# Kernel optimization log

Measured on AMD Instinct MI355X. Metric: run time of the kernel, lower is better.

Reference implementation:

```python
import jax, jax.numpy as jnp
import numpy as np

# NF4 codebook (bitsandbytes nf4 quant_type), 16 levels in [-1, 1]
NF4 = jnp.array([
    -1.0, -0.6961928009986877, -0.5250730514526367, -0.39491748809814453,
    -0.28444138169288635, -0.18477343022823334, -0.09105003625154495, 0.0,
    0.07958029955625534, 0.16093020141124725, 0.24611230194568634,
    0.33791524171829224, 0.44070982933044434, 0.5626170039176941,
    0.7229568362236023, 1.0], dtype=jnp.float32)
BLOCK = 64  # bitsandbytes default quant block size

TOKENS, HD, M = 8192, 4096, 11008


def dequant_nf4(codes, scales):
    # codes: [out, in] int in [0,16); scales: [out, in//BLOCK] per-block absmax
    out_f, in_f = codes.shape
    w = NF4[codes].reshape(out_f, in_f // BLOCK, BLOCK) * scales[:, :, None]
    return w.reshape(out_f, in_f)


def setup_inputs() -> dict:
    key = jax.random.key(0)
    k = jax.random.split(key, 7)
    return {
        "x": jax.random.normal(k[0], (TOKENS, HD), dtype=jnp.float32),
        "gate_codes": jax.random.randint(k[1], (M, HD), 0, 16, dtype=jnp.int32),
        "gate_scales": jax.random.uniform(k[2], (M, HD // BLOCK), dtype=jnp.float32) * 0.1,
        "up_codes": jax.random.randint(k[3], (M, HD), 0, 16, dtype=jnp.int32),
        "up_scales": jax.random.uniform(k[4], (M, HD // BLOCK), dtype=jnp.float32) * 0.1,
        "down_codes": jax.random.randint(k[5], (HD, M), 0, 16, dtype=jnp.int32),
        "down_scales": jax.random.uniform(k[6], (HD, M // BLOCK), dtype=jnp.float32) * 0.1,
    }


def reference(x, gate_codes, gate_scales, up_codes, up_scales, down_codes, down_scales):
    Wg = dequant_nf4(gate_codes, gate_scales)   # [m, hd]
    Wu = dequant_nf4(up_codes, up_scales)       # [m, hd]
    Wd = dequant_nf4(down_codes, down_scales)   # [hd, m]
    g = jnp.einsum('td,md->tm', x, Wg)          # gate_proj(x)
    u = jnp.einsum('td,md->tm', x, Wu)          # up_proj(x)
    h = jax.nn.silu(g) * u                      # SwiGLU
    return jnp.einsum('tm,dm->td', h, Wd)       # down_proj
```

## Files before the change

### kernel.cpp

```cpp
#include <hip/hip_runtime.h>
#include <hip/hip_bf16.h>

typedef _Float16 half8 __attribute__((ext_vector_type(8)));
typedef float floatx4 __attribute__((ext_vector_type(4)));

__device__ __constant__ float NF4_TAB[16] = {
    -1.0f, -0.6961928009986877f, -0.5250730514526367f, -0.39491748809814453f,
    -0.28444138169288635f, -0.18477343022823334f, -0.09105003625154495f, 0.0f,
    0.07958029955625534f, 0.16093020141124725f, 0.24611230194568634f,
    0.33791524171829224f, 0.44070982933044434f, 0.5626170039176941f,
    0.7229568362236023f, 1.0f};

typedef __attribute__((address_space(3))) void lds_t;
typedef __attribute__((address_space(1))) void gbl_t;

__device__ __forceinline__ void gload16(const void* g, void* l) {
  __builtin_amdgcn_global_load_lds((gbl_t*)g, (lds_t*)l, 16, 0, 0);
}

#define FENCE() asm volatile("" ::: "memory")

__global__ void cvt_f32_to_f16_pad(const float* __restrict__ in,
                                   _Float16* __restrict__ out,
                                   int total8, int C8, int OS) {
  int stride = gridDim.x * blockDim.x;
  for (int i = blockIdx.x * blockDim.x + threadIdx.x; i < total8; i += stride) {
    int row = i / C8;
    int col = (i - row * C8) * 8;
    const float4* ip = reinterpret_cast<const float4*>(in + (long)row * (C8 * 8) + col);
    float4 a = ip[0], b = ip[1];
    half8 o;
    o[0] = (_Float16)a.x; o[1] = (_Float16)a.y;
    o[2] = (_Float16)a.z; o[3] = (_Float16)a.w;
    o[4] = (_Float16)b.x; o[5] = (_Float16)b.y;
    o[6] = (_Float16)b.z; o[7] = (_Float16)b.w;
    *reinterpret_cast<half8*>(out + (long)row * OS + col) = o;
  }
}

__global__ void dequant_nf4(const int* __restrict__ codes,
                            const float* __restrict__ scales,
                            _Float16* __restrict__ out,
                            int total8, int C, int CB, int OS) {
  __shared__ float lut[16];
  if (threadIdx.x < 16) lut[threadIdx.x] = NF4_TAB[threadIdx.x];
  __syncthreads();
  int stride = gridDim.x * blockDim.x;
  for (int i = blockIdx.x * blockDim.x + threadIdx.x; i < total8; i += stride) {
    long e = (long)i * 8;
    int row = (int)(e / C);
    int col = (int)(e - (long)row * C);
    float sc = scales[row * CB + (col >> 6)];
    const int4* cp = reinterpret_cast<const int4*>(codes + e);
    int4 c0 = cp[0];
    int4 c1 = cp[1];
    half8 o;
    o[0] = (_Float16)(lut[c0.x & 15] * sc);
    o[1] = (_Float16)(lut[c0.y & 15] * sc);
    o[2] = (_Float16)(lut[c0.z & 15] * sc);
    o[3] = (_Float16)(lut[c0.w & 15] * sc);
    o[4] = (_Float16)(lut[c1.x & 15] * sc);
    o[5] = (_Float16)(lut[c1.y & 15] * sc);
    o[6] = (_Float16)(lut[c1.z & 15] * sc);
    o[7] = (_Float16)(lut[c1.w & 15] * sc);
    *reinterpret_cast<half8*>(out + (long)row * OS + col) = o;
  }
}

template <int K, int LD, int N, int EPI>
__global__ __launch_bounds__(512, 2) void gemm256(
    const _Float16* __restrict__ A,
    const _Float16* __restrict__ B,
    _Float16* __restrict__ GH,
    float* __restrict__ OUT) {
  constexpr int NT = K / 64;
  constexpr int NBC = N / 256;
  __shared__ __align__(16) _Float16 lds[2 * 32768];

  const int t = threadIdx.x;
  const int lane = t & 63;
  const int wave = t >> 6;
  const int wm = wave >> 2;
  const int wn = wave & 3;

  const int xcd = blockIdx.x & 7;
  const int j = blockIdx.x >> 3;
  const int bm = 4 * xcd + (j & 3);
  const int bn = j >> 2;

  const int lc = (t & 3) ^ ((t >> 3) & 3);
  const _Float16* gA = A + ((long)bm * 256 + (t >> 2)) * LD + lc * 8;
  const _Float16* gB = B + ((long)bn * 256 + (t >> 2)) * LD + lc * 8;
  const long rstep = (long)128 * LD;
  const int dst = t * 8;

  const int rA = wm * 128 + (lane & 15);
  const int rB = wn * 64 + (lane & 15);
  const int ckA = ((lane >> 4) ^ ((rA >> 1) & 3)) * 8;
  const int ckB = ((lane >> 4) ^ ((rB >> 1) & 3)) * 8;
  const int offA = rA * 32 + ckA;
  const int offB = 16384 + rB * 32 + ckB;

#define STAGE_SLOT(gp, slab, koff, dbuf)                                   \
  gload16((gp) + (koff), lds + (dbuf) * 32768 + (slab) + dst);             \
  gload16((gp) + (koff) + rstep, lds + (dbuf) * 32768 + (slab) + dst + 4096);

  STAGE_SLOT(gA, 0, 0, 0);
  STAGE_SLOT(gB, 16384, 0, 0);
  STAGE_SLOT(gA, 8192, 32, 0);
  STAGE_SLOT(gB, 24576, 32, 0);
  gA += 64; gB += 64;
  asm volatile("s_waitcnt vmcnt(4)" ::: "memory");
  __builtin_amdgcn_s_barrier();
  FENCE();

  floatx4 acc[8][4] = {};

  for (int kt = 0; kt < NT; ++kt) {
    const int cb = kt & 1;
    const int sbuf = cb ^ 1;
    const _Float16* lb = lds + cb * 32768;
    const bool st = (kt + 1 < NT);
    const bool last = (kt == NT - 1);

    half8 a[8], b[2];

#pragma unroll
    for (int i = 0; i < 8; ++i)
      a[i] = *reinterpret_cast<const half8*>(&lb[offA + i * 512]);
    b[0] = *reinterpret_cast<const half8*>(&lb[offB]);
    b[1] = *reinterpret_cast<const half8*>(&lb[offB + 512]);
    if (st) { STAGE_SLOT(gA, 0, 0, sbuf); }
    __builtin_amdgcn_s_barrier();
    FENCE();
    __builtin_amdgcn_s_setprio(1);
#pragma unroll
    for (int i = 0; i < 8; ++i) {
      acc[i][0] = __builtin_amdgcn_mfma_f32_16x16x32_f16(a[i], b[0], acc[i][0], 0, 0, 0);
      acc[i][1] = __builtin_amdgcn_mfma_f32_16x16x32_f16(a[i], b[1], acc[i][1], 0, 0, 0);
    }
    __builtin_amdgcn_s_setprio(0);
    __builtin_amdgcn_s_barrier();
    FENCE();

    b[0] = *reinterpret_cast<const half8*>(&lb[offB + 2 * 512]);
    b[1] = *reinterpret_cast<const half8*>(&lb[offB + 3 * 512]);
    if (st) { STAGE_SLOT(gB, 16384, 0, sbuf); }
    if (last) { asm volatile("s_waitcnt vmcnt(0)" ::: "memory"); }
    else      { asm volatile("s_waitcnt vmcnt(4)" ::: "memory"); }
    __builtin_amdgcn_s_barrier();
    FENCE();
    __builtin_amdgcn_s_setprio(1);
#pragma unroll
    for (int i = 0; i < 8; ++i) {
      acc[i][2] = __builtin_amdgcn_mfma_f32_16x16x32_f16(a[i], b[0], acc[i][2], 0, 0, 0);
      acc[i][3] = __builtin_amdgcn_mfma_f32_16x16x32_f16(a[i], b[1], acc[i][3], 0, 0, 0);
    }
    __builtin_amdgcn_s_setprio(0);
    __builtin_amdgcn_s_barrier();
    FENCE();

#pragma unroll
    for (int i = 0; i < 8; ++i)
      a[i] = *reinterpret_cast<const half8*>(&lb[8192 + offA + i * 512]);
    b[0] = *reinterpret_cast<const half8*>(&lb[8192 + offB]);
    b[1] = *reinterpret_cast<const half8*>(&lb[8192 + offB + 512]);
    if (st) { STAGE_SLOT(gA, 8192, 32, sbuf); }
    __builtin_amdgcn_s_barrier();
    FENCE();
    __builtin_amdgcn_s_setprio(1);
#pragma unroll
    for (int i = 0; i < 8; ++i) {
      acc[i][0] = __builtin_amdgcn_mfma_f32_16x16x32_f16(a[i], b[0], acc[i][0], 0, 0, 0);
      acc[i][1] = __builtin_amdgcn_mfma_f32_16x16x32_f16(a[i], b[1], acc[i][1], 0, 0, 0);
    }
    __builtin_amdgcn_s_setprio(0);
    __builtin_amdgcn_s_barrier();
    FENCE();

    b[0] = *reinterpret_cast<const half8*>(&lb[8192 + offB + 2 * 512]);
    b[1] = *reinterpret_cast<const half8*>(&lb[8192 + offB + 3 * 512]);
    if (st) { STAGE_SLOT(gB, 24576, 32, sbuf); gA += 64; gB += 64; }
    if (!last) { asm volatile("s_waitcnt vmcnt(4)" ::: "memory"); }
    __builtin_amdgcn_s_barrier();
    FENCE();
    __builtin_amdgcn_s_setprio(1);
#pragma unroll
    for (int i = 0; i < 8; ++i) {
      acc[i][2] = __builtin_amdgcn_mfma_f32_16x16x32_f16(a[i], b[0], acc[i][2], 0, 0, 0);
      acc[i][3] = __builtin_amdgcn_mfma_f32_16x16x32_f16(a[i], b[1], acc[i][3], 0, 0, 0);
    }
    __builtin_amdgcn_s_setprio(0);
    __builtin_amdgcn_s_barrier();
    FENCE();
  }
#undef STAGE_SLOT

  const int r0 = bm * 256 + wm * 128 + (lane >> 4) * 4;
  const int c0 = bn * 256 + wn * 64 + (lane & 15);

  if (EPI == 1) {
    _Float16* lg = lds;
    const _Float16* gsrc = GH + (long)(bm * 256) * N + bn * 256;
#pragma unroll
    for (int r = 0; r < 16; ++r) {
      const int row = r * 16 + (t >> 5);
      const int col = (t & 31) * 8;
      gload16(gsrc + (long)row * N + col, lg + r * 4096 + t * 8);
    }
    asm volatile("s_waitcnt vmcnt(0)" ::: "memory");
    __builtin_amdgcn_s_barrier();
    FENCE();
    const int lr0 = wm * 128 + (lane >> 4) * 4;
    const int lc0 = wn * 64 + (lane & 15);
#pragma unroll
    for (int i = 0; i < 8; ++i) {
#pragma unroll
      for (int j2 = 0; j2 < 4; ++j2) {
#pragma unroll
        for (int ii = 0; ii < 4; ++ii) {
          const long idx = (long)(r0 + i * 16 + ii) * N + (c0 + j2 * 16);
          float u = acc[i][j2][ii];
          float g = (float)lg[(lr0 + i * 16 + ii) * 256 + (lc0 + j2 * 16)];
          GH[idx] = (_Float16)(g / (1.0f + __expf(-g)) * u);
        }
      }
    }
  } else {
#pragma unroll
    for (int i = 0; i < 8; ++i) {
#pragma unroll
      for (int j2 = 0; j2 < 4; ++j2) {
#pragma unroll
        for (int ii = 0; ii < 4; ++ii) {
          const long idx = (long)(r0 + i * 16 + ii) * N + (c0 + j2 * 16);
          if (EPI == 0) {
            GH[idx] = (_Float16)acc[i][j2][ii];
          } else {
            OUT[idx] = acc[i][j2][ii];
          }
        }
      }
    }
  }
}

extern "C" void kernel_launch(void* const* d_in, const int* in_sizes, int n_in,
                              void* d_out, int out_size, void* d_ws, size_t ws_size,
                              hipStream_t stream) {
  const float* x           = (const float*)d_in[0];
  const int*   gate_codes  = (const int*)d_in[1];
  const float* gate_scales = (const float*)d_in[2];
  const int*   up_codes    = (const int*)d_in[3];
  const float* up_scales   = (const float*)d_in[4];
  const int*   down_codes  = (const int*)d_in[5];
  const float* down_scales = (const float*)d_in[6];
  float* out = (float*)d_out;

  const long T = 8192, HD = 4096, M = 11008;
  const long LDP = 4160;

  char* ws = (char*)d_ws;
  _Float16* x16 = (_Float16*)ws;
  _Float16* W   = (_Float16*)(ws + T * LDP * 2);
  _Float16* gh  = (_Float16*)(ws + T * LDP * 2 + M * LDP * 2);

  cvt_f32_to_f16_pad<<<2048, 256, 0, stream>>>(x, x16, (int)(T * HD / 8),
                                               (int)(HD / 8), (int)LDP);

  dequant_nf4<<<2048, 256, 0, stream>>>(gate_codes, gate_scales, W,
                                        (int)(M * HD / 8), (int)HD, (int)(HD / 64),
                                        (int)LDP);
  gemm256<4096, 4160, 11008, 0><<<(8192 / 256) * (11008 / 256), 512, 0, stream>>>(
      x16, W, gh, nullptr);

  dequant_nf4<<<2048, 256, 0, stream>>>(up_codes, up_scales, W,
                                        (int)(M * HD / 8), (int)HD, (int)(HD / 64),
                                        (int)LDP);
  gemm256<4096, 4160, 11008, 1><<<(8192 / 256) * (11008 / 256), 512, 0, stream>>>(
      x16, W, gh, nullptr);

  dequant_nf4<<<2048, 256, 0, stream>>>(down_codes, down_scales, W,
                                        (int)(HD * M / 8), (int)M, (int)(M / 64),
                                        (int)M);
  gemm256<11008, 11008, 4096, 2><<<(8192 / 256) * (4096 / 256), 512, 0, stream>>>(
      gh, W, nullptr, out);
}
```

Baseline: 2.225 ms.

## Fuse gate and up projections into one dual-accumulator GEMM with SwiGLU epilogue

Replaces the separate gate GEMM (writing fp16 g to global) and the up GEMM (which reloaded g in its epilogue) with one kernel. It stages a shared A tile plus 128-column tiles of both Wg and Wu and keeps two accumulator sets, then applies SiLU(g)*u in registers. This removes a full pass over x and the intermediate g write/read. It also drops the padded 4160 leading dimension in favour of an unpadded 4096, which may increase LDS or cache conflicts, and requires buffers for both dequantized weights at once.

```diff
diff --git a/kernel.cpp b/kernel.cpp
--- a/kernel.cpp
+++ b/kernel.cpp
@@ -67,6 +67,158 @@
   }
 }
 
+template <int K, int LD, int N>
+__global__ __launch_bounds__(512, 2) void gemm_fused(
+    const _Float16* __restrict__ A,
+    const _Float16* __restrict__ G,
+    const _Float16* __restrict__ U,
+    _Float16* __restrict__ GH) {
+  constexpr int NT = K / 64;
+  __shared__ __align__(16) _Float16 lds[2 * 32768];
+
+  const int t = threadIdx.x;
+  const int lane = t & 63;
+  const int wave = t >> 6;
+  const int wm = wave >> 2;
+  const int wn = wave & 3;
+
+  const int xcd = blockIdx.x & 7;
+  const int j = blockIdx.x >> 3;
+  const int bm = 4 * xcd + (j & 3);
+  const int bn = j >> 2;
+
+  const int lc = (t & 3) ^ ((t >> 3) & 3);
+  const _Float16* gA = A + ((long)bm * 256 + (t >> 2)) * LD + lc * 8;
+  const _Float16* gG = G + ((long)bn * 128 + (t >> 2)) * LD + lc * 8;
+  const _Float16* gU = U + ((long)bn * 128 + (t >> 2)) * LD + lc * 8;
+  const long rstep = (long)128 * LD;
+  const int dst = t * 8;
+
+  const int rA = wm * 128 + (lane & 15);
+  const int rB = wn * 32 + (lane & 15);
+  const int ckA = ((lane >> 4) ^ ((rA >> 1) & 3)) * 8;
+  const int ckB = ((lane >> 4) ^ ((rB >> 1) & 3)) * 8;
+  const int offA = rA * 32 + ckA;
+  const int offBG = 16384 + rB * 32 + ckB;
+  const int offBU = 24576 + rB * 32 + ckB;
+
+  gload16(gA, lds + dst);
+  gload16(gA + rstep, lds + dst + 4096);
+  gload16(gG, lds + 16384 + dst);
+  gload16(gU, lds + 24576 + dst);
+  gload16(gA + 32, lds + 8192 + dst);
+  gload16(gA + 32 + rstep, lds + 8192 + dst + 4096);
+  gload16(gG + 32, lds + 20480 + dst);
+  gload16(gU + 32, lds + 28672 + dst);
+  gA += 64; gG += 64; gU += 64;
+  asm volatile("s_waitcnt vmcnt(4)" ::: "memory");
+  __builtin_amdgcn_s_barrier();
+  FENCE();
+
+  floatx4 accG[8][2] = {};
+  floatx4 accU[8][2] = {};
+
+  for (int kt = 0; kt < NT; ++kt) {
+    const int cb = kt & 1;
+    const int sbuf = cb ^ 1;
+    const _Float16* lb = lds + cb * 32768;
+    _Float16* sb = lds + sbuf * 32768;
+    const bool st = (kt + 1 < NT);
+    const bool last = (kt == NT - 1);
+
+    half8 a[8], b[2];
+
+#pragma unroll
+    for (int i = 0; i < 8; ++i)
+      a[i] = *reinterpret_cast<const half8*>(&lb[offA + i * 512]);
+    b[0] = *reinterpret_cast<const half8*>(&lb[offBG]);
+    b[1] = *reinterpret_cast<const half8*>(&lb[offBG + 512]);
+    if (st) { gload16(gA, sb + dst); gload16(gA + rstep, sb + dst + 4096); }
+    __builtin_amdgcn_s_barrier();
+    FENCE();
+    __builtin_amdgcn_s_setprio(1);
+#pragma unroll
+    for (int i = 0; i < 8; ++i) {
+      accG[i][0] = __builtin_amdgcn_mfma_f32_16x16x32_f16(a[i], b[0], accG[i][0], 0, 0, 0);
+      accG[i][1] = __builtin_amdgcn_mfma_f32_16x16x32_f16(a[i], b[1], accG[i][1], 0, 0, 0);
+    }
+    __builtin_amdgcn_s_setprio(0);
+    __builtin_amdgcn_s_barrier();
+    FENCE();
+
+    b[0] = *reinterpret_cast<const half8*>(&lb[offBU]);
+    b[1] = *reinterpret_cast<const half8*>(&lb[offBU + 512]);
+    if (st) { gload16(gG, sb + 16384 + dst); gload16(gU, sb + 24576 + dst); }
+    if (last) { asm volatile("s_waitcnt vmcnt(0)" ::: "memory"); }
+    else      { asm volatile("s_waitcnt vmcnt(4)" ::: "memory"); }
+    __builtin_amdgcn_s_barrier();
+    FENCE();
+    __builtin_amdgcn_s_setprio(1);
+#pragma unroll
+    for (int i = 0; i < 8; ++i) {
+      accU[i][0] = __builtin_amdgcn_mfma_f32_16x16x32_f16(a[i], b[0], accU[i][0], 0, 0, 0);
+      accU[i][1] = __builtin_amdgcn_mfma_f32_16x16x32_f16(a[i], b[1], accU[i][1], 0, 0, 0);
+    }
+    __builtin_amdgcn_s_setprio(0);
+    __builtin_amdgcn_s_barrier();
+    FENCE();
+
+#pragma unroll
+    for (int i = 0; i < 8; ++i)
+      a[i] = *reinterpret_cast<const half8*>(&lb[8192 + offA + i * 512]);
+    b[0] = *reinterpret_cast<const half8*>(&lb[offBG + 4096]);
+    b[1] = *reinterpret_cast<const half8*>(&lb[offBG + 4096 + 512]);
+    if (st) { gload16(gA + 32, sb + 8192 + dst); gload16(gA + 32 + rstep, sb + 8192 + dst + 4096); }
+    __builtin_amdgcn_s_barrier();
+    FENCE();
+    __builtin_amdgcn_s_setprio(1);
+#pragma unroll
+    for (int i = 0; i < 8; ++i) {
+      accG[i][0] = __builtin_amdgcn_mfma_f32_16x16x32_f16(a[i], b[0], accG[i][0], 0, 0, 0);
+      accG[i][1] = __builtin_amdgcn_mfma_f32_16x16x32_f16(a[i], b[1], accG[i][1], 0, 0, 0);
+    }
+    __builtin_amdgcn_s_setprio(0);
+    __builtin_amdgcn_s_barrier();
+    FENCE();
+
+    b[0] = *reinterpret_cast<const half8*>(&lb[offBU + 4096]);
+    b[1] = *reinterpret_cast<const half8*>(&lb[offBU + 4096 + 512]);
+    if (st) {
+      gload16(gG + 32, sb + 20480 + dst);
+      gload16(gU + 32, sb + 28672 + dst);
+      gA += 64; gG += 64; gU += 64;
+    }
+    if (!last) { asm volatile("s_waitcnt vmcnt(4)" ::: "memory"); }
+    __builtin_amdgcn_s_barrier();
+    FENCE();
+    __builtin_amdgcn_s_setprio(1);
+#pragma unroll
+    for (int i = 0; i < 8; ++i) {
+      accU[i][0] = __builtin_amdgcn_mfma_f32_16x16x32_f16(a[i], b[0], accU[i][0], 0, 0, 0);
+      accU[i][1] = __builtin_amdgcn_mfma_f32_16x16x32_f16(a[i], b[1], accU[i][1], 0, 0, 0);
+    }
+    __builtin_amdgcn_s_setprio(0);
+    __builtin_amdgcn_s_barrier();
+    FENCE();
+  }
+
+  const int r0 = bm * 256 + wm * 128 + (lane >> 4) * 4;
+  const int c0 = bn * 128 + wn * 32 + (lane & 15);
+#pragma unroll
+  for (int i = 0; i < 8; ++i) {
+#pragma unroll
+    for (int j2 = 0; j2 < 2; ++j2) {
+#pragma unroll
+      for (int ii = 0; ii < 4; ++ii) {
+        const long idx = (long)(r0 + i * 16 + ii) * N + (c0 + j2 * 16);
+        float g = accG[i][j2][ii];
+        float u = accU[i][j2][ii];
+        GH[idx] = (_Float16)(g / (1.0f + __expf(-g)) * u);
+      }
+    }
+  }
+}
+
 template <int K, int LD, int N, int EPI>
 __global__ __launch_bounds__(512, 2) void gemm256(
     const _Float16* __restrict__ A,
@@ -198,47 +350,17 @@
 
   const int r0 = bm * 256 + wm * 128 + (lane >> 4) * 4;
   const int c0 = bn * 256 + wn * 64 + (lane & 15);
-
-  if (EPI == 1) {
-    _Float16* lg = lds;
-    const _Float16* gsrc = GH + (long)(bm * 256) * N + bn * 256;
-#pragma unroll
-    for (int r = 0; r < 16; ++r) {
-      const int row = r * 16 + (t >> 5);
-      const int col = (t & 31) * 8;
-      gload16(gsrc + (long)row * N + col, lg + r * 4096 + t * 8);
-    }
-    asm volatile("s_waitcnt vmcnt(0)" ::: "memory");
-    __builtin_amdgcn_s_barrier();
-    FENCE();
-    const int lr0 = wm * 128 + (lane >> 4) * 4;
-    const int lc0 = wn * 64 + (lane & 15);
-#pragma unroll
-    for (int i = 0; i < 8; ++i) {
-#pragma unroll
-      for (int j2 = 0; j2 < 4; ++j2) {
-#pragma unroll
-        for (int ii = 0; ii < 4; ++ii) {
-          const long idx = (long)(r0 + i * 16 + ii) * N + (c0 + j2 * 16);
-          float u = acc[i][j2][ii];
-          float g = (float)lg[(lr0 + i * 16 + ii) * 256 + (lc0 + j2 * 16)];
-          GH[idx] = (_Float16)(g / (1.0f + __expf(-g)) * u);
-        }
-      }
-    }
-  } else {
-#pragma unroll
-    for (int i = 0; i < 8; ++i) {
-#pragma unroll
-      for (int j2 = 0; j2 < 4; ++j2) {
-#pragma unroll
-        for (int ii = 0; ii < 4; ++ii) {
-          const long idx = (long)(r0 + i * 16 + ii) * N + (c0 + j2 * 16);
-          if (EPI == 0) {
-            GH[idx] = (_Float16)acc[i][j2][ii];
-          } else {
-            OUT[idx] = acc[i][j2][ii];
-          }
+#pragma unroll
+  for (int i = 0; i < 8; ++i) {
+#pragma unroll
+    for (int j2 = 0; j2 < 4; ++j2) {
+#pragma unroll
+      for (int ii = 0; ii < 4; ++ii) {
+        const long idx = (long)(r0 + i * 16 + ii) * N + (c0 + j2 * 16);
+        if (EPI == 0) {
+          GH[idx] = (_Float16)acc[i][j2][ii];
+        } else {
+          OUT[idx] = acc[i][j2][ii];
         }
       }
     }
@@ -258,31 +380,28 @@
   float* out = (float*)d_out;
 
   const long T = 8192, HD = 4096, M = 11008;
-  const long LDP = 4160;
 
   char* ws = (char*)d_ws;
   _Float16* x16 = (_Float16*)ws;
-  _Float16* W   = (_Float16*)(ws + T * LDP * 2);
-  _Float16* gh  = (_Float16*)(ws + T * LDP * 2 + M * LDP * 2);
+  _Float16* Wg  = (_Float16*)(ws + T * HD * 2);
+  _Float16* Wu  = (_Float16*)(ws + T * HD * 2 + M * HD * 2);
+  _Float16* gh  = (_Float16*)(ws + T * HD * 2 + 2 * M * HD * 2);
 
   cvt_f32_to_f16_pad<<<2048, 256, 0, stream>>>(x, x16, (int)(T * HD / 8),
-                                               (int)(HD / 8), (int)LDP);
-
-  dequant_nf4<<<2048, 256, 0, stream>>>(gate_codes, gate_scales, W,
+                                               (int)(HD / 8), (int)HD);
+  dequant_nf4<<<2048, 256, 0, stream>>>(gate_codes, gate_scales, Wg,
                                         (int)(M * HD / 8), (int)HD, (int)(HD / 64),
-                                        (int)LDP);
-  gemm256<4096, 4160, 11008, 0><<<(8192 / 256) * (11008 / 256), 512, 0, stream>>>(
-      x16, W, gh, nullptr);
-
-  dequant_nf4<<<2048, 256, 0, stream>>>(up_codes, up_scales, W,
+                                        (int)HD);
+  dequant_nf4<<<2048, 256, 0, stream>>>(up_codes, up_scales, Wu,
                                         (int)(M * HD / 8), (int)HD, (int)(HD / 64),
-                                        (int)LDP);
-  gemm256<4096, 4160, 11008, 1><<<(8192 / 256) * (11008 / 256), 512, 0, stream>>>(
-      x16, W, gh, nullptr);
-
-  dequant_nf4<<<2048, 256, 0, stream>>>(down_codes, down_scales, W,
+                                        (int)HD);
+
+  gemm_fused<4096, 4096, 11008><<<(8192 / 256) * (11008 / 128), 512, 0, stream>>>(
+      x16, Wg, Wu, gh);
+
+  dequant_nf4<<<2048, 256, 0, stream>>>(down_codes, down_scales, Wg,
                                         (int)(HD * M / 8), (int)M, (int)(M / 64),
                                         (int)M);
   gemm256<11008, 11008, 4096, 2><<<(8192 / 256) * (4096 / 256), 512, 0, stream>>>(
-      gh, W, nullptr, out);
-}
+      gh, Wg, nullptr, out);
+}
```

Measured after the change: 2.114 ms (median of 2 runs). 5.0% less time.
